# Kernel tuning notes

Hardware: AMD Instinct MI355X
Metric: run time of the kernel (lower is better)

Reference implementation:

```python
import jax, jax.numpy as jnp
import numpy as np

D_MODEL = 2048
N_HEADS = 16
HEAD_DIM = 128
WINDOW = 256
B, T = 2, 2048
SCALE = float(np.sqrt(HEAD_DIM))


def setup_inputs() -> dict:
    key = jax.random.key(0)
    ks = jax.random.split(key, 5)
    init = 0.02
    x = jax.random.normal(ks[0], (B, T, D_MODEL), dtype=jnp.float32)
    Wq = jax.random.normal(ks[1], (D_MODEL, D_MODEL), dtype=jnp.float32) * init
    Wk = jax.random.normal(ks[2], (D_MODEL, D_MODEL), dtype=jnp.float32) * init
    Wv = jax.random.normal(ks[3], (D_MODEL, D_MODEL), dtype=jnp.float32) * init
    Wo = jax.random.normal(ks[4], (D_MODEL, D_MODEL), dtype=jnp.float32) * init
    return {"x": x, "Wq": Wq, "Wk": Wk, "Wv": Wv, "Wo": Wo}


def _allowed_mask():
    # [H, T, T] bool: global (even) heads -> causal; local (odd) heads -> causal band of WINDOW
    idx = jnp.arange(T)
    causal = idx[None, :] <= idx[:, None]                      # [T, T]
    band = idx[None, :] >= (idx[:, None] - WINDOW + 1)         # [T, T]
    is_global = (jnp.arange(N_HEADS) % 2) == 0                 # [H]
    return causal[None] & (is_global[:, None, None] | band[None])


def reference(x, Wq, Wk, Wv, Wo):
    # projections (nn.Linear: y = x @ W.T), reshape to [B, H, T, D]
    def proj(W):
        return (x @ W.T).reshape(B, T, N_HEADS, HEAD_DIM).transpose(0, 2, 1, 3)

    q, k, v = proj(Wq), proj(Wk), proj(Wv)
    scores = jnp.einsum("bhtd,bhsd->bhts", q, k) / SCALE       # [B, H, T, T]
    allowed = _allowed_mask()                                  # [H, T, T]
    neg_inf = jnp.asarray(-jnp.inf, dtype=scores.dtype)
    scores = jnp.where(allowed[None], scores, neg_inf)
    attn = jax.nn.softmax(scores, axis=-1)
    out = jnp.einsum("bhts,bhsd->bhtd", attn, v)               # [B, H, T, D]
    concat = out.transpose(0, 2, 1, 3).reshape(B, T, N_HEADS * HEAD_DIM)
    return concat @ Wo.T
```

## Files before the change

kernel.cpp:

```cpp
#include <hip/hip_runtime.h>

typedef __attribute__((ext_vector_type(4))) float f32x4;
typedef __attribute__((ext_vector_type(8))) short bf16x8;
typedef __attribute__((ext_vector_type(4))) unsigned short u16x4;
typedef unsigned short u16;

#define MFMA16(a, b, c) __builtin_amdgcn_mfma_f32_16x16x32_bf16((a), (b), (c), 0, 0, 0)

#define T_SEQ 2048
#define DMODEL 2048
#define NHEADS 16
#define HDIM 128
#define WINDOW 256
#define MROWS 4096
#define SC 0.08838834764831845f

__device__ __forceinline__ u16 f2bf(float f) {
  union { float f; unsigned u; } v; v.f = f;
  return (u16)((v.u + 0x7FFFu + ((v.u >> 16) & 1u)) >> 16);
}
__device__ __forceinline__ float bf2f(u16 u) {
  union { unsigned u; float f; } v; v.u = ((unsigned)u) << 16;
  return v.f;
}
__device__ __forceinline__ void gl_lds16(const u16* g, u16* l) {
  __builtin_amdgcn_global_load_lds((const __attribute__((address_space(1))) void*)(g),
                                   (__attribute__((address_space(3))) void*)(l), 16, 0, 0);
}

#define BAR __builtin_amdgcn_s_barrier()
#define FEN asm volatile("" ::: "memory")
#define VMC3 asm volatile("s_waitcnt vmcnt(3)" ::: "memory")
#define VMC2 asm volatile("s_waitcnt vmcnt(2)" ::: "memory")
#define VMC0 asm volatile("s_waitcnt vmcnt(0)" ::: "memory")

__global__ __launch_bounds__(256) void convert_all(const float* __restrict__ x,
                                                   const float* __restrict__ wq,
                                                   const float* __restrict__ wk,
                                                   const float* __restrict__ wv,
                                                   const float* __restrict__ wo,
                                                   u16* __restrict__ dst) {
  const size_t NX = (size_t)MROWS * DMODEL;
  const size_t NW = (size_t)DMODEL * DMODEL;
  const size_t chunks = (NX + 4 * NW) / 8;
  for (size_t ci = (size_t)blockIdx.x * 256 + threadIdx.x; ci < chunks;
       ci += (size_t)gridDim.x * 256) {
    const size_t off = ci * 8;
    const float* src;
    size_t so;
    if (off < NX) { src = x; so = off; }
    else {
      size_t rem = off - NX;
      if (rem < NW) { src = wq; so = rem; }
      else if (rem < 2 * NW) { src = wk; so = rem - NW; }
      else if (rem < 3 * NW) { src = wv; so = rem - 2 * NW; }
      else { src = wo; so = rem - 3 * NW; }
    }
    f32x4 a = *(const f32x4*)&src[so];
    f32x4 b = *(const f32x4*)&src[so + 4];
    bf16x8 o;
#pragma unroll
    for (int j = 0; j < 4; ++j) { o[j] = (short)f2bf(a[j]); o[j + 4] = (short)f2bf(b[j]); }
    *(bf16x8*)&dst[off] = o;
  }
}

__global__ __launch_bounds__(512, 2) void gemm_qkv(const u16* __restrict__ A,
                                                   const u16* __restrict__ W,
                                                   u16* __restrict__ qk,
                                                   u16* __restrict__ vt) {
  __shared__ u16 lds[57344];
  const int tid = threadIdx.x, w = tid >> 6, lane = tid & 63;
  const int wm = w >> 2, wn = w & 3;
  const int fr = lane & 15, g = lane >> 4, g4 = g * 4;

  const int xcd = blockIdx.x & 7, bi = blockIdx.x >> 3;
  const int mt = bi >> 2, nt = xcd * 4 + (bi & 3);
  const int m0 = mt * 256, n0 = nt * 192;

  const int xs0 = (g ^ (fr & 7)) * 8;
  const int xs1 = xs0 ^ 32;
  const int aRow = wm * 128 + fr;
  const int bRow = wn * 48 + fr;

  const int sr = tid >> 3;
  const int scc = ((tid & 7) ^ (sr & 7)) * 8;
  const u16* pA0  = A + (size_t)(m0 + sr) * DMODEL + scc;
  const u16* pA1  = A + (size_t)(m0 + 64 + sr) * DMODEL + scc;
  const u16* pB0  = W + (size_t)(n0 + sr) * DMODEL + scc;
  const u16* pB0b = W + (size_t)(n0 + 64 + sr) * DMODEL + scc;
  const u16* pB1  = W + (size_t)(n0 + 128 + sr) * DMODEL + scc;

#define SAH(h, t, c)                                                                   \
  { gl_lds16(pA0 + (size_t)(h) * 128 * DMODEL + (t) * 64,                              \
             &lds[(c) * 16384 + (h) * 8192 + w * 512]);                                \
    gl_lds16(pA1 + (size_t)(h) * 128 * DMODEL + (t) * 64,                              \
             &lds[(c) * 16384 + (h) * 8192 + 4096 + w * 512]); }
#define SBH0(t, c)                                                                     \
  { gl_lds16(pB0 + (size_t)(t) * 64, &lds[32768 + (c) * 12288 + w * 512]);             \
    gl_lds16(pB0b + (size_t)(t) * 64, &lds[32768 + (c) * 12288 + 4096 + w * 512]); }
#define SBH1(t, c)                                                                     \
  { gl_lds16(pB1 + (size_t)(t) * 64, &lds[32768 + (c) * 12288 + 8192 + w * 512]); }

#define RD_AL(c)                                                                       \
  { _Pragma("unroll") for (int m_ = 0; m_ < 4; ++m_) {                                 \
      af[m_][0] = *(const bf16x8*)&lds[(c) * 16384 + (aRow + m_ * 16) * 64 + xs0];     \
      af[m_][1] = *(const bf16x8*)&lds[(c) * 16384 + (aRow + m_ * 16) * 64 + xs1]; } }
#define RD_AH(c)                                                                       \
  { _Pragma("unroll") for (int m_ = 0; m_ < 4; ++m_) {                                 \
      af[m_][0] = *(const bf16x8*)&lds[(c) * 16384 + (aRow + 64 + m_ * 16) * 64 + xs0];\
      af[m_][1] = *(const bf16x8*)&lds[(c) * 16384 + (aRow + 64 + m_ * 16) * 64 + xs1]; } }
#define RD_B(c)                                                                        \
  { _Pragma("unroll") for (int n_ = 0; n_ < 3; ++n_) {                                 \
      bfr[n_][0] = *(const bf16x8*)&lds[32768 + (c) * 12288 + (bRow + n_ * 16) * 64 + xs0]; \
      bfr[n_][1] = *(const bf16x8*)&lds[32768 + (c) * 12288 + (bRow + n_ * 16) * 64 + xs1]; } }

#define MMQ(MB)                                                                        \
  { __builtin_amdgcn_s_setprio(1);                                                    \
    _Pragma("unroll") for (int kc_ = 0; kc_ < 2; ++kc_)                                \
      _Pragma("unroll") for (int m_ = 0; m_ < 4; ++m_)                                 \
        _Pragma("unroll") for (int n_ = 0; n_ < 3; ++n_)                               \
          acc[(MB) + m_][n_] = MFMA16(af[m_][kc_], bfr[n_][kc_], acc[(MB) + m_][n_]);  \
    __builtin_amdgcn_s_setprio(0); }

  bf16x8 af[4][2], bfr[3][2];
  f32x4 acc[8][3];
#pragma unroll
  for (int i = 0; i < 8; ++i)
#pragma unroll
    for (int j = 0; j < 3; ++j) acc[i][j] = (f32x4){0.f, 0.f, 0.f, 0.f};

  SAH(0, 0, 0); SAH(1, 0, 0);
  SBH0(0, 0); SBH1(0, 0);
  SBH0(1, 1); SBH1(1, 1);
  VMC3; BAR;

#pragma unroll 1
  for (int i = 0; i < 15; ++i) {
    const int t0 = 2 * i;
    RD_AL(0); RD_B(0); SAH(0, t0 + 1, 1); SAH(1, t0 + 1, 1);
    FEN; BAR; MMQ(0); FEN; BAR;
    RD_AH(0); SBH0(t0 + 2, 0); SBH1(t0 + 2, 0);
    VMC3; BAR; MMQ(4); FEN; BAR;
    RD_AL(1); RD_B(1); SAH(0, t0 + 2, 0); SAH(1, t0 + 2, 0);
    FEN; BAR; MMQ(0); FEN; BAR;
    RD_AH(1); SBH0(t0 + 3, 1); SBH1(t0 + 3, 1);
    VMC3; BAR; MMQ(4); FEN; BAR;
  }
  RD_AL(0); RD_B(0); SAH(0, 31, 1); SAH(1, 31, 1);
  FEN; BAR; MMQ(0); FEN; BAR;
  RD_AH(0);
  VMC0; BAR; MMQ(4); FEN; BAR;
  RD_AL(1); RD_B(1);
  FEN; BAR; MMQ(0); FEN; BAR;
  RD_AH(1);
  FEN; BAR; MMQ(4);

#pragma unroll
  for (int mi = 0; mi < 8; ++mi)
#pragma unroll
    for (int ni = 0; ni < 3; ++ni) {
      const int row0 = m0 + wm * 128 + mi * 16 + g4;
      const int cg = n0 + wn * 48 + ni * 16 + fr;
      if (cg < 2 * DMODEL) {
#pragma unroll
        for (int r = 0; r < 4; ++r)
          qk[(size_t)(row0 + r) * (2 * DMODEL) + cg] = f2bf(acc[mi][ni][r]);
      } else {
        const int cc = cg - 2 * DMODEL;
        const int hh = cc >> 7, d = cc & 127;
        const int bb = row0 >> 11, tl = row0 & 2047;
        u16x4 w4;
#pragma unroll
        for (int r = 0; r < 4; ++r) w4[r] = f2bf(acc[mi][ni][r]);
        *(u16x4*)&vt[((size_t)(bb * NHEADS + hh) * HDIM + d) * T_SEQ + tl] = w4;
      }
    }
#undef SAH
#undef SBH0
#undef SBH1
#undef RD_AL
#undef RD_AH
#undef RD_B
#undef MMQ
}

__global__ __launch_bounds__(512, 2) void gemm_out(const u16* __restrict__ A,
                                                   const u16* __restrict__ W0,
                                                   float* __restrict__ outf) {
  __shared__ u16 lds2[49152];
  const int tid = threadIdx.x, w = tid >> 6, lane = tid & 63;
  const int wm = w >> 2, wn = w & 3;
  const int fr = lane & 15, g = lane >> 4, g4 = g * 4;

  const int xcd = blockIdx.x & 7, bi = blockIdx.x >> 3;
  const int mt = bi >> 1, nt = xcd * 2 + (bi & 1);
  const int m0 = mt * 256, n0 = nt * 128;

  const int xs0 = (g ^ (fr & 7)) * 8;
  const int xs1 = xs0 ^ 32;
  const int aRow = wm * 128 + fr;
  const int bRow = wn * 32 + fr;

  const int sr = tid >> 3;
  const int scc = ((tid & 7) ^ (sr & 7)) * 8;
  const u16* pA0  = A + (size_t)(m0 + sr) * DMODEL + scc;
  const u16* pA1  = A + (size_t)(m0 + 64 + sr) * DMODEL + scc;
  const u16* pB0  = W0 + (size_t)(n0 + sr) * DMODEL + scc;
  const u16* pB0b = W0 + (size_t)(n0 + 64 + sr) * DMODEL + scc;

#define S2A(h, t, c)                                                                   \
  { gl_lds16(pA0 + (size_t)(h) * 128 * DMODEL + (t) * 64,                              \
             &lds2[(c) * 16384 + (h) * 8192 + w * 512]);                               \
    gl_lds16(pA1 + (size_t)(h) * 128 * DMODEL + (t) * 64,                              \
             &lds2[(c) * 16384 + (h) * 8192 + 4096 + w * 512]); }
#define S2B(t, c)                                                                      \
  { gl_lds16(pB0 + (size_t)(t) * 64, &lds2[32768 + (c) * 8192 + w * 512]);             \
    gl_lds16(pB0b + (size_t)(t) * 64, &lds2[32768 + (c) * 8192 + 4096 + w * 512]); }

#define R2AL(c)                                                                        \
  { _Pragma("unroll") for (int m_ = 0; m_ < 4; ++m_) {                                 \
      af[m_][0] = *(const bf16x8*)&lds2[(c) * 16384 + (aRow + m_ * 16) * 64 + xs0];    \
      af[m_][1] = *(const bf16x8*)&lds2[(c) * 16384 + (aRow + m_ * 16) * 64 + xs1]; } }
#define R2AH(c)                                                                        \
  { _Pragma("unroll") for (int m_ = 0; m_ < 4; ++m_) {                                 \
      af[m_][0] = *(const bf16x8*)&lds2[(c) * 16384 + (aRow + 64 + m_ * 16) * 64 + xs0]; \
      af[m_][1] = *(const bf16x8*)&lds2[(c) * 16384 + (aRow + 64 + m_ * 16) * 64 + xs1]; } }
#define R2B(c)                                                                         \
  { _Pragma("unroll") for (int n_ = 0; n_ < 2; ++n_) {                                 \
      bfr[n_][0] = *(const bf16x8*)&lds2[32768 + (c) * 8192 + (bRow + n_ * 16) * 64 + xs0]; \
      bfr[n_][1] = *(const bf16x8*)&lds2[32768 + (c) * 8192 + (bRow + n_ * 16) * 64 + xs1]; } }

#define M2(MB)                                                                         \
  { __builtin_amdgcn_s_setprio(1);                                                    \
    _Pragma("unroll") for (int kc_ = 0; kc_ < 2; ++kc_)                                \
      _Pragma("unroll") for (int m_ = 0; m_ < 4; ++m_)                                 \
        _Pragma("unroll") for (int n_ = 0; n_ < 2; ++n_)                               \
          acc[(MB) + m_][n_] = MFMA16(af[m_][kc_], bfr[n_][kc_], acc[(MB) + m_][n_]);  \
    __builtin_amdgcn_s_setprio(0); }

  bf16x8 af[4][2], bfr[2][2];
  f32x4 acc[8][2];
#pragma unroll
  for (int i = 0; i < 8; ++i)
#pragma unroll
    for (int j = 0; j < 2; ++j) acc[i][j] = (f32x4){0.f, 0.f, 0.f, 0.f};

  S2A(0, 0, 0); S2A(1, 0, 0);
  S2B(0, 0);
  S2B(1, 1);
  VMC2; BAR;

#pragma unroll 1
  for (int i = 0; i < 15; ++i) {
    const int t0 = 2 * i;
    R2AL(0); R2B(0); S2A(0, t0 + 1, 1); S2A(1, t0 + 1, 1);
    FEN; BAR; M2(0); FEN; BAR;
    R2AH(0); S2B(t0 + 2, 0);
    VMC2; BAR; M2(4); FEN; BAR;
    R2AL(1); R2B(1); S2A(0, t0 + 2, 0); S2A(1, t0 + 2, 0);
    FEN; BAR; M2(0); FEN; BAR;
    R2AH(1); S2B(t0 + 3, 1);
    VMC2; BAR; M2(4); FEN; BAR;
  }
  R2AL(0); R2B(0); S2A(0, 31, 1); S2A(1, 31, 1);
  FEN; BAR; M2(0); FEN; BAR;
  R2AH(0);
  VMC0; BAR; M2(4); FEN; BAR;
  R2AL(1); R2B(1);
  FEN; BAR; M2(0); FEN; BAR;
  R2AH(1);
  FEN; BAR; M2(4);

#pragma unroll
  for (int mi = 0; mi < 8; ++mi)
#pragma unroll
    for (int ni = 0; ni < 2; ++ni) {
      const int row0 = m0 + wm * 128 + mi * 16 + g4;
      const int c = n0 + wn * 32 + ni * 16 + fr;
#pragma unroll
      for (int r = 0; r < 4; ++r)
        outf[(size_t)(row0 + r) * DMODEL + c] = acc[mi][ni][r];
    }
#undef S2A
#undef S2B
#undef R2AL
#undef R2AH
#undef R2B
#undef M2
}

#define QB 64
#define KVB 64
#define LDK 136
#define LDV 72
#define LDP 80

__global__ __launch_bounds__(256) void attn_kernel(const u16* __restrict__ qk,
                                                   const u16* __restrict__ vt,
                                                   u16* __restrict__ op,
                                                   u16* __restrict__ pO,
                                                   float* __restrict__ pm,
                                                   float* __restrict__ pl) {
  __shared__ u16 Ks[KVB][LDK];
  __shared__ u16 Vs[HDIM][LDV];
  __shared__ u16 Ps[4][16][LDP];

  const int bx = blockIdx.x, h = blockIdx.y, b = blockIdx.z;
  const bool isglobal = (h & 1) == 0;
  int qt, klo, khi, part = 0;
  bool partial = false;
  if (isglobal) {
    const int c = 47 - bx;
    if (c < 16) { qt = c; klo = 0; khi = qt; }
    else {
      qt = 16 + ((c - 16) >> 1);
      part = (c - 16) & 1;
      partial = true;
      if (part == 0) { klo = 0; khi = 15; } else { klo = 16; khi = qt; }
    }
  } else {
    if (bx >= 32) return;
    qt = 31 - bx;
    const int lo_ = qt * QB - (WINDOW - 1);
    klo = lo_ > 0 ? (lo_ >> 6) : 0;
    khi = qt;
  }

  const int tid = threadIdx.x, wave = tid >> 6, lane = tid & 63;
  const int fr = lane & 15, ko = (lane >> 4) * 8, g4 = (lane >> 4) * 4;
  const int q0 = qt * QB;
  const size_t baseq = (size_t)b * T_SEQ * (2 * DMODEL) + (size_t)h * HDIM;
  const size_t basek = baseq + DMODEL;
  const size_t basev = (size_t)(b * NHEADS + h) * HDIM * T_SEQ;
  const size_t baseo = (size_t)b * T_SEQ * DMODEL + (size_t)h * HDIM;

  bf16x8 qf[4];
  {
    const int qrow = q0 + wave * 16 + fr;
#pragma unroll
    for (int ds = 0; ds < 4; ++ds)
      qf[ds] = *(const bf16x8*)&qk[baseq + (size_t)qrow * (2 * DMODEL) + ds * 32 + ko];
  }

  float mrun = -1e30f, lrun = 0.f;
  f32x4 o[8];
#pragma unroll
  for (int dt = 0; dt < 8; ++dt) o[dt] = (f32x4){0.f, 0.f, 0.f, 0.f};

  const int kr = tid >> 4, kc = (tid & 15) * 8;
  const int vr = tid >> 3, vc = (tid & 7) * 8;
  bf16x8 kreg[4], vreg[4];

#define LOADTILE(KT)                                                                      \
  {                                                                                       \
    _Pragma("unroll") for (int it = 0; it < 4; ++it) {                                    \
      kreg[it] = *(const bf16x8*)&qk[basek + (size_t)((KT) * KVB + kr + it * 16) * (2 * DMODEL) + kc]; \
      vreg[it] = *(const bf16x8*)&vt[basev + (size_t)(vr + it * 32) * T_SEQ + (KT) * KVB + vc];        \
    }                                                                                     \
  }
#define WRITETILE()                                                                       \
  {                                                                                       \
    _Pragma("unroll") for (int it = 0; it < 4; ++it) {                                    \
      *(bf16x8*)&Ks[kr + it * 16][kc] = kreg[it];                                         \
      *(bf16x8*)&Vs[vr + it * 32][vc] = vreg[it];                                         \
    }                                                                                     \
  }

  LOADTILE(klo);
  WRITETILE();
  __syncthreads();

  const int qg = q0 + wave * 16 + fr;

  for (int kt = klo; kt <= khi; ++kt) {
    const bool more = kt < khi;
    if (more) LOADTILE(kt + 1);

    f32x4 s[4];
    __builtin_amdgcn_s_setprio(1);
#pragma unroll
    for (int kk = 0; kk < 4; ++kk) {
      f32x4 a = (f32x4){0.f, 0.f, 0.f, 0.f};
#pragma unroll
      for (int ds = 0; ds < 4; ++ds) {
        bf16x8 kf = *(const bf16x8*)&Ks[kk * 16 + fr][ds * 32 + ko];
        a = MFMA16(kf, qf[ds], a);
      }
      s[kk] = a;
    }
    __builtin_amdgcn_s_setprio(0);

    float sv[16];
    float pmax = -1e30f;
#pragma unroll
    for (int kk = 0; kk < 4; ++kk)
#pragma unroll
      for (int reg = 0; reg < 4; ++reg) {
        const int cg = kt * KVB + kk * 16 + g4 + reg;
        const bool allowed = (cg <= qg) && (isglobal || cg >= qg - (WINDOW - 1));
        const float v = allowed ? s[kk][reg] : -1e30f;
        sv[kk * 4 + reg] = v;
        pmax = fmaxf(pmax, v);
      }
    pmax = fmaxf(pmax, __shfl_xor(pmax, 16, 64));
    pmax = fmaxf(pmax, __shfl_xor(pmax, 32, 64));
    const float nm = fmaxf(mrun, pmax);
    const float fac = __expf((mrun - nm) * SC);
    mrun = nm;
    float rs = 0.f;
    u16 pb[16];
#pragma unroll
    for (int i = 0; i < 16; ++i) {
      const float p = (sv[i] > -5e29f) ? __expf((sv[i] - nm) * SC) : 0.f;
      rs += p;
      pb[i] = f2bf(p);
    }
    rs += __shfl_xor(rs, 16, 64);
    rs += __shfl_xor(rs, 32, 64);
    lrun = lrun * fac + rs;

#pragma unroll
    for (int kk = 0; kk < 4; ++kk) {
      u16x4 w;
      w[0] = pb[kk * 4]; w[1] = pb[kk * 4 + 1]; w[2] = pb[kk * 4 + 2]; w[3] = pb[kk * 4 + 3];
      *(u16x4*)&Ps[wave][fr][kk * 16 + g4] = w;
    }

    float ff[4];
#pragma unroll
    for (int r = 0; r < 4; ++r) ff[r] = __shfl(fac, g4 + r, 64);
#pragma unroll
    for (int dt = 0; dt < 8; ++dt)
#pragma unroll
      for (int r = 0; r < 4; ++r) o[dt][r] *= ff[r];

    bf16x8 pf0 = *(const bf16x8*)&Ps[wave][fr][ko];
    bf16x8 pf1 = *(const bf16x8*)&Ps[wave][fr][32 + ko];
    __builtin_amdgcn_s_setprio(1);
#pragma unroll
    for (int dt = 0; dt < 8; ++dt) {
      bf16x8 vf0 = *(const bf16x8*)&Vs[dt * 16 + fr][ko];
      bf16x8 vf1 = *(const bf16x8*)&Vs[dt * 16 + fr][32 + ko];
      o[dt] = MFMA16(pf0, vf0, o[dt]);
      o[dt] = MFMA16(pf1, vf1, o[dt]);
    }
    __builtin_amdgcn_s_setprio(0);

    __syncthreads();
    if (more) WRITETILE();
    __syncthreads();
  }

  if (!partial) {
    const float inv = 1.0f / lrun;
    float iv[4];
#pragma unroll
    for (int r = 0; r < 4; ++r) iv[r] = __shfl(inv, g4 + r, 64);
#pragma unroll
    for (int r = 0; r < 4; ++r) {
      const int qrow = q0 + wave * 16 + g4 + r;
#pragma unroll
      for (int dt = 0; dt < 8; ++dt)
        op[baseo + (size_t)qrow * DMODEL + dt * 16 + fr] = f2bf(o[dt][r] * iv[r]);
    }
  } else {
    const int sidx = (((b * 8 + (h >> 1)) * 16 + (qt - 16)) << 1) + part;
    const size_t sb = (size_t)sidx * 64;
#pragma unroll
    for (int r = 0; r < 4; ++r) {
      const size_t row = sb + wave * 16 + g4 + r;
#pragma unroll
      for (int dt = 0; dt < 8; ++dt)
        pO[row * HDIM + dt * 16 + fr] = f2bf(o[dt][r]);
    }
    if (lane < 16) {
      pm[sb + wave * 16 + lane] = mrun;
      pl[sb + wave * 16 + lane] = lrun;
    }
  }
}

__global__ __launch_bounds__(256) void merge_kernel(const u16* __restrict__ pO,
                                                    const float* __restrict__ pm,
                                                    const float* __restrict__ pl,
                                                    u16* __restrict__ op) {
  const int x = blockIdx.x;
  const int qt16 = x & 15, eh = (x >> 4) & 7, b = x >> 7;
  const int h = eh * 2, qt = 16 + qt16;
  const int s0 = x * 2, s1 = s0 + 1;

  for (int i = 0; i < 4; ++i) {
    const int vidx = threadIdx.x + i * 256;
    const int row = vidx >> 4, d8 = (vidx & 15) * 8;
    const float m0 = pm[s0 * 64 + row], m1 = pm[s1 * 64 + row];
    const float l0 = pl[s0 * 64 + row], l1 = pl[s1 * 64 + row];
    const float m = fmaxf(m0, m1);
    const float w0 = __expf((m0 - m) * SC), w1 = __expf((m1 - m) * SC);
    const float inv = 1.0f / (l0 * w0 + l1 * w1);
    bf16x8 a = *(const bf16x8*)&pO[((size_t)s0 * 64 + row) * HDIM + d8];
    bf16x8 c = *(const bf16x8*)&pO[((size_t)s1 * 64 + row) * HDIM + d8];
    bf16x8 r;
#pragma unroll
    for (int j = 0; j < 8; ++j)
      r[j] = (short)f2bf((bf2f((u16)a[j]) * w0 + bf2f((u16)c[j]) * w1) * inv);
    *(bf16x8*)&op[((size_t)(b * T_SEQ + qt * 64 + row)) * DMODEL + h * HDIM + d8] = r;
  }
}

extern "C" void kernel_launch(void* const* d_in, const int* in_sizes, int n_in,
                              void* d_out, int out_size, void* d_ws, size_t ws_size,
                              hipStream_t stream) {
  (void)in_sizes; (void)n_in; (void)out_size; (void)ws_size;
  const float* x  = (const float*)d_in[0];
  const float* Wq = (const float*)d_in[1];
  const float* Wk = (const float*)d_in[2];
  const float* Wv = (const float*)d_in[3];
  const float* Wo = (const float*)d_in[4];

  const size_t NX = (size_t)MROWS * DMODEL;
  const size_t NW = (size_t)DMODEL * DMODEL;
  u16* ws  = (u16*)d_ws;
  u16* xb  = ws;
  u16* wqb = ws + NX;
  u16* wkb = wqb + NW;
  u16* wvb = wkb + NW;
  u16* wob = wvb + NW;
  u16* qkb = wob + NW;
  u16* vtb = qkb + (size_t)MROWS * 2 * DMODEL;

  u16*   pO = wqb;
  float* pm = (float*)(wqb + (size_t)512 * 64 * HDIM);
  float* pl = pm + 512 * 64;

  convert_all<<<2048, 256, 0, stream>>>(x, Wq, Wk, Wv, Wo, ws);

  gemm_qkv<<<512, 512, 0, stream>>>(xb, wqb, qkb, vtb);

  attn_kernel<<<dim3(48, NHEADS, 2), 256, 0, stream>>>(qkb, vtb, xb, pO, pm, pl);

  merge_kernel<<<256, 256, 0, stream>>>(pO, pm, pl, xb);

  gemm_out<<<256, 512, 0, stream>>>(xb, wob, (float*)d_out);
}
```

Before: 256.9 us.

## Double attention query tile to 128 rows with eight waves per block

Raises the attention query block from 64 to 128 rows and runs 8 waves (512 threads) per block, so each loaded K/V tile is reused by twice as many query rows. The global-head split schedule, local-window tile ranges, partial-result indexing and the merge kernel are all remapped to the new tile size. This halves K/V global traffic and the block count per query, at the cost of fewer, larger blocks, coarser load balance and a longer causal tail per block.

```diff
diff --git a/kernel.cpp b/kernel.cpp
--- a/kernel.cpp
+++ b/kernel.cpp
@@ -290,13 +290,13 @@
 #undef M2
 }
 
-#define QB 64
+#define QB 128
 #define KVB 64
 #define LDK 136
 #define LDV 72
 #define LDP 80
 
-__global__ __launch_bounds__(256) void attn_kernel(const u16* __restrict__ qk,
+__global__ __launch_bounds__(512) void attn_kernel(const u16* __restrict__ qk,
                                                    const u16* __restrict__ vt,
                                                    u16* __restrict__ op,
                                                    u16* __restrict__ pO,
@@ -304,27 +304,28 @@
                                                    float* __restrict__ pl) {
   __shared__ u16 Ks[KVB][LDK];
   __shared__ u16 Vs[HDIM][LDV];
-  __shared__ u16 Ps[4][16][LDP];
+  __shared__ u16 Ps[8][16][LDP];
 
   const int bx = blockIdx.x, h = blockIdx.y, b = blockIdx.z;
   const bool isglobal = (h & 1) == 0;
   int qt, klo, khi, part = 0;
   bool partial = false;
   if (isglobal) {
-    const int c = 47 - bx;
-    if (c < 16) { qt = c; klo = 0; khi = qt; }
-    else {
-      qt = 16 + ((c - 16) >> 1);
-      part = (c - 16) & 1;
+    if (bx < 16) {
+      qt = 15 - (bx >> 1);
+      part = bx & 1;
       partial = true;
-      if (part == 0) { klo = 0; khi = 15; } else { klo = 16; khi = qt; }
+      if (part == 0) { klo = 0; khi = 15; } else { klo = 16; khi = 2 * qt + 1; }
+    } else {
+      qt = 23 - bx;
+      klo = 0; khi = 2 * qt + 1;
     }
   } else {
-    if (bx >= 32) return;
-    qt = 31 - bx;
+    if (bx >= 16) return;
+    qt = 15 - bx;
     const int lo_ = qt * QB - (WINDOW - 1);
     klo = lo_ > 0 ? (lo_ >> 6) : 0;
-    khi = qt;
+    khi = 2 * qt + 1;
   }
 
   const int tid = threadIdx.x, wave = tid >> 6, lane = tid & 63;
@@ -350,20 +351,20 @@
 
   const int kr = tid >> 4, kc = (tid & 15) * 8;
   const int vr = tid >> 3, vc = (tid & 7) * 8;
-  bf16x8 kreg[4], vreg[4];
+  bf16x8 kreg[2], vreg[2];
 
 #define LOADTILE(KT)                                                                      \
   {                                                                                       \
-    _Pragma("unroll") for (int it = 0; it < 4; ++it) {                                    \
-      kreg[it] = *(const bf16x8*)&qk[basek + (size_t)((KT) * KVB + kr + it * 16) * (2 * DMODEL) + kc]; \
-      vreg[it] = *(const bf16x8*)&vt[basev + (size_t)(vr + it * 32) * T_SEQ + (KT) * KVB + vc];        \
+    _Pragma("unroll") for (int it = 0; it < 2; ++it) {                                    \
+      kreg[it] = *(const bf16x8*)&qk[basek + (size_t)((KT) * KVB + kr + it * 32) * (2 * DMODEL) + kc]; \
+      vreg[it] = *(const bf16x8*)&vt[basev + (size_t)(vr + it * 64) * T_SEQ + (KT) * KVB + vc];        \
     }                                                                                     \
   }
 #define WRITETILE()                                                                       \
   {                                                                                       \
-    _Pragma("unroll") for (int it = 0; it < 4; ++it) {                                    \
-      *(bf16x8*)&Ks[kr + it * 16][kc] = kreg[it];                                         \
-      *(bf16x8*)&Vs[vr + it * 32][vc] = vreg[it];                                         \
+    _Pragma("unroll") for (int it = 0; it < 2; ++it) {                                    \
+      *(bf16x8*)&Ks[kr + it * 32][kc] = kreg[it];                                         \
+      *(bf16x8*)&Vs[vr + it * 64][vc] = vreg[it];                                         \
     }                                                                                     \
   }
 
@@ -422,9 +423,9 @@
 
 #pragma unroll
     for (int kk = 0; kk < 4; ++kk) {
-      u16x4 w;
-      w[0] = pb[kk * 4]; w[1] = pb[kk * 4 + 1]; w[2] = pb[kk * 4 + 2]; w[3] = pb[kk * 4 + 3];
-      *(u16x4*)&Ps[wave][fr][kk * 16 + g4] = w;
+      u16x4 wv;
+      wv[0] = pb[kk * 4]; wv[1] = pb[kk * 4 + 1]; wv[2] = pb[kk * 4 + 2]; wv[3] = pb[kk * 4 + 3];
+      *(u16x4*)&Ps[wave][fr][kk * 16 + g4] = wv;
     }
 
     float ff[4];
@@ -465,8 +466,8 @@
         op[baseo + (size_t)qrow * DMODEL + dt * 16 + fr] = f2bf(o[dt][r] * iv[r]);
     }
   } else {
-    const int sidx = (((b * 8 + (h >> 1)) * 16 + (qt - 16)) << 1) + part;
-    const size_t sb = (size_t)sidx * 64;
+    const int sidx = (((b * 8 + (h >> 1)) * 8 + (qt - 8)) << 1) + part;
+    const size_t sb = (size_t)sidx * QB;
 #pragma unroll
     for (int r = 0; r < 4; ++r) {
       const size_t row = sb + wave * 16 + g4 + r;
@@ -486,25 +487,26 @@
                                                     const float* __restrict__ pl,
                                                     u16* __restrict__ op) {
   const int x = blockIdx.x;
-  const int qt16 = x & 15, eh = (x >> 4) & 7, b = x >> 7;
-  const int h = eh * 2, qt = 16 + qt16;
+  if (x >= 128) return;
+  const int qt8 = x & 7, eh = (x >> 3) & 7, b = x >> 6;
+  const int h = eh * 2, qt = 8 + qt8;
   const int s0 = x * 2, s1 = s0 + 1;
 
-  for (int i = 0; i < 4; ++i) {
+  for (int i = 0; i < 8; ++i) {
     const int vidx = threadIdx.x + i * 256;
     const int row = vidx >> 4, d8 = (vidx & 15) * 8;
-    const float m0 = pm[s0 * 64 + row], m1 = pm[s1 * 64 + row];
-    const float l0 = pl[s0 * 64 + row], l1 = pl[s1 * 64 + row];
+    const float m0 = pm[s0 * QB + row], m1 = pm[s1 * QB + row];
+    const float l0 = pl[s0 * QB + row], l1 = pl[s1 * QB + row];
     const float m = fmaxf(m0, m1);
     const float w0 = __expf((m0 - m) * SC), w1 = __expf((m1 - m) * SC);
     const float inv = 1.0f / (l0 * w0 + l1 * w1);
-    bf16x8 a = *(const bf16x8*)&pO[((size_t)s0 * 64 + row) * HDIM + d8];
-    bf16x8 c = *(const bf16x8*)&pO[((size_t)s1 * 64 + row) * HDIM + d8];
+    bf16x8 a = *(const bf16x8*)&pO[((size_t)s0 * QB + row) * HDIM + d8];
+    bf16x8 c = *(const bf16x8*)&pO[((size_t)s1 * QB + row) * HDIM + d8];
     bf16x8 r;
 #pragma unroll
     for (int j = 0; j < 8; ++j)
       r[j] = (short)f2bf((bf2f((u16)a[j]) * w0 + bf2f((u16)c[j]) * w1) * inv);
-    *(bf16x8*)&op[((size_t)(b * T_SEQ + qt * 64 + row)) * DMODEL + h * HDIM + d8] = r;
+    *(bf16x8*)&op[((size_t)(b * T_SEQ + qt * QB + row)) * DMODEL + h * HDIM + d8] = r;
   }
 }
 
@@ -530,16 +532,16 @@
   u16* vtb = qkb + (size_t)MROWS * 2 * DMODEL;
 
   u16*   pO = wqb;
-  float* pm = (float*)(wqb + (size_t)512 * 64 * HDIM);
-  float* pl = pm + 512 * 64;
+  float* pm = (float*)(wqb + (size_t)256 * QB * HDIM);
+  float* pl = pm + 256 * QB;
 
   convert_all<<<2048, 256, 0, stream>>>(x, Wq, Wk, Wv, Wo, ws);
 
   gemm_qkv<<<512, 512, 0, stream>>>(xb, wqb, qkb, vtb);
 
-  attn_kernel<<<dim3(48, NHEADS, 2), 256, 0, stream>>>(qkb, vtb, xb, pO, pm, pl);
-
-  merge_kernel<<<256, 256, 0, stream>>>(pO, pm, pl, xb);
+  attn_kernel<<<dim3(24, NHEADS, 2), 512, 0, stream>>>(qkb, vtb, xb, pO, pm, pl);
+
+  merge_kernel<<<128, 256, 0, stream>>>(pO, pm, pl, xb);
 
   gemm_out<<<256, 512, 0, stream>>>(xb, wob, (float*)d_out);
 }
```

Result: no change. 258.8 us (+0.8%).
